# Optimization experiments

Hardware: AMD Instinct MI355X
Metric: run time of the kernel (lower is better)

The kernel has to match this reference:

```python
import jax, jax.numpy as jnp
import numpy as np

B, DK, N, DV = 16, 64, 8192, 64


def setup_inputs() -> dict:
    key = jax.random.key(0)
    kq, kk, kv = jax.random.split(key, 3)
    q = jax.random.normal(kq, (B, DK, N), dtype=jnp.float32)   # channel-first q
    k = jax.random.normal(kk, (B, N, DK), dtype=jnp.float32)
    v = jax.random.normal(kv, (B, N, DV), dtype=jnp.float32)
    return {"q": q, "k": k, "v": v}


def reference(q, k, v):
    # torch: bmm(q.permute(0,2,1), bmm(k.permute(0,2,1), v))
    # k^T v: [B, DK, DV] -- small on-chip-able intermediate
    ktv = jnp.einsum('bnk,bnv->bkv', k, v)
    # q^T (k^T v): [B, N, DV]
    out = jnp.einsum('bkn,bkv->bnv', q, ktv)
    return out
```

## Files before the change

### kernel.cpp

```cpp
#include <hip/hip_runtime.h>


#define B_   16
#define N_   8192
#define DK_  64
#define DV_  64
#define CH_  32

__global__ __launch_bounds__(256) void p1_partial(
    const float* __restrict__ K, const float* __restrict__ V,
    float* __restrict__ part)
{
    __shared__ float sm[4][4096];

    const int c = blockIdx.x, b = blockIdx.y, t = threadIdx.x;
    const int w = t >> 6, lane = t & 63;
    const int kk = (lane >> 3) * 8;
    const int vv = (lane & 7) * 8;

    float* Ks = &sm[w][0];
    float* Vs = &sm[w][2048];

    const size_t row0 = (size_t)b * N_ + (size_t)c * 256 + (size_t)w * 64;
    const float4* K4 = (const float4*)(K + row0 * DK_);
    const float4* V4 = (const float4*)(V + row0 * DV_);

    float acc[8][8] = {};

    for (int r = 0; r < 2; ++r) {
        #pragma unroll
        for (int j = 0; j < 8; ++j) {
            ((float4*)Ks)[lane + 64 * j] = K4[r * 512 + lane + 64 * j];
            ((float4*)Vs)[lane + 64 * j] = V4[r * 512 + lane + 64 * j];
        }
        #pragma unroll 4
        for (int n = 0; n < 32; ++n) {
            alignas(16) float fk[8], fv[8];
            *(float4*)&fk[0] = *(const float4*)&Ks[n * 64 + kk];
            *(float4*)&fk[4] = *(const float4*)&Ks[n * 64 + kk + 4];
            *(float4*)&fv[0] = *(const float4*)&Vs[n * 64 + vv];
            *(float4*)&fv[4] = *(const float4*)&Vs[n * 64 + vv + 4];
            #pragma unroll
            for (int i = 0; i < 8; ++i)
                #pragma unroll
                for (int j = 0; j < 8; ++j)
                    acc[i][j] += fk[i] * fv[j];
        }
    }

    float* reg = sm[w];
    #pragma unroll
    for (int i = 0; i < 8; ++i) {
        *(float4*)&reg[(kk + i) * 64 + vv]     = make_float4(acc[i][0], acc[i][1], acc[i][2], acc[i][3]);
        *(float4*)&reg[(kk + i) * 64 + vv + 4] = make_float4(acc[i][4], acc[i][5], acc[i][6], acc[i][7]);
    }
    __syncthreads();

    float4* P = (float4*)(part + ((size_t)c * B_ + b) * 4096);
    #pragma unroll
    for (int j = 0; j < 4; ++j) {
        const int idx = t + 256 * j;
        const float4 s0 = ((const float4*)sm[0])[idx];
        const float4 s1 = ((const float4*)sm[1])[idx];
        const float4 s2 = ((const float4*)sm[2])[idx];
        const float4 s3 = ((const float4*)sm[3])[idx];
        P[idx] = make_float4(s0.x + s1.x + s2.x + s3.x,
                             s0.y + s1.y + s2.y + s3.y,
                             s0.z + s1.z + s2.z + s3.z,
                             s0.w + s1.w + s2.w + s3.w);
    }
}

__global__ __launch_bounds__(256) void p1_reduce(
    const float* __restrict__ part, float* __restrict__ ktv)
{
    const int idx = blockIdx.x * 256 + threadIdx.x;
    float s = 0.f;
    #pragma unroll
    for (int c = 0; c < CH_; ++c)
        s += part[(size_t)c * 65536 + idx];
    ktv[idx] = s;
}

__global__ __launch_bounds__(256) void p2(
    const float* __restrict__ q, const float* __restrict__ ktv,
    float* __restrict__ out)
{
    __shared__ float ks[4096];
    __shared__ float qs[4][4096];

    const int nb = blockIdx.x, b = blockIdx.y, t = threadIdx.x;
    const int w = t >> 6, lane = t & 63;
    const int nl = (lane >> 3) * 8;
    const int vl = (lane & 7) * 8;
    const int n0 = nb * 256 + w * 64;

    const float4* kt4 = (const float4*)(ktv + (size_t)b * 4096);
    #pragma unroll
    for (int j = 0; j < 4; ++j)
        ((float4*)ks)[t + 256 * j] = kt4[t + 256 * j];

    const float* qb = q + (size_t)b * DK_ * N_ + n0;
    #pragma unroll
    for (int j = 0; j < 16; ++j) {
        const int idx = lane + 64 * j;
        ((float4*)qs[w])[idx] =
            ((const float4*)(qb + (size_t)(idx >> 4) * N_))[idx & 15];
    }
    __syncthreads();

    float acc[8][8] = {};
    #pragma unroll 8
    for (int k = 0; k < 64; ++k) {
        alignas(16) float fq[8], fv[8];
        *(float4*)&fq[0] = *(const float4*)&qs[w][k * 64 + nl];
        *(float4*)&fq[4] = *(const float4*)&qs[w][k * 64 + nl + 4];
        *(float4*)&fv[0] = *(const float4*)&ks[k * 64 + vl];
        *(float4*)&fv[4] = *(const float4*)&ks[k * 64 + vl + 4];
        #pragma unroll
        for (int i = 0; i < 8; ++i)
            #pragma unroll
            for (int j = 0; j < 8; ++j)
                acc[i][j] += fq[i] * fv[j];
    }

    float* ob = out + ((size_t)b * N_ + n0 + nl) * DV_ + vl;
    #pragma unroll
    for (int i = 0; i < 8; ++i) {
        *(float4*)&ob[(size_t)i * DV_]     = make_float4(acc[i][0], acc[i][1], acc[i][2], acc[i][3]);
        *(float4*)&ob[(size_t)i * DV_ + 4] = make_float4(acc[i][4], acc[i][5], acc[i][6], acc[i][7]);
    }
}

extern "C" void kernel_launch(void* const* d_in, const int* in_sizes, int n_in,
                              void* d_out, int out_size, void* d_ws, size_t ws_size,
                              hipStream_t stream)
{
    (void)in_sizes; (void)n_in; (void)out_size; (void)ws_size;
    const float* q = (const float*)d_in[0];
    const float* k = (const float*)d_in[1];
    const float* v = (const float*)d_in[2];
    float* out = (float*)d_out;

    float* part = (float*)d_ws;
    float* ktv  = part + (size_t)CH_ * B_ * 4096;

    p1_partial<<<dim3(CH_, B_), 256, 0, stream>>>(k, v, part);
    p1_reduce<<<dim3(256), 256, 0, stream>>>(part, ktv);
    p2<<<dim3(32, B_), 256, 0, stream>>>(q, ktv, out);
}
```

Measured before the change: 151.7 us.

## Use direct global-to-LDS loads with double buffering to overlap loads and FMA

Replaces register-staged global-to-shared copies with global_load_lds DMA builtins in both the K^T V partial kernel and the q-projection kernel. The partial kernel is split into four 16-row chunks with two LDS buffers, so the next chunk's loads are issued while the current one is computed. In p2 the second half of q is loaded after the barrier and overlaps the first half of the k-loop. The goal is to hide global memory latency and free registers. Correctness now relies on manual vmcnt waits and on the fixed per-lane LDS placement of the DMA builtin, which is fragile.

Result: no change. 152.3 us (+0.4%).

```diff
diff --git a/kernel.cpp b/kernel.cpp
--- a/kernel.cpp
+++ b/kernel.cpp
@@ -6,6 +6,13 @@
 #define DK_  64
 #define DV_  64
 #define CH_  32
+
+__device__ __forceinline__ void dma16(const void* g, void* l) {
+    __builtin_amdgcn_global_load_lds(
+        (const __attribute__((address_space(1))) void*)g,
+        (__attribute__((address_space(3))) void*)l, 16, 0, 0);
+}
+#define WAITVM(n) __builtin_amdgcn_s_waitcnt(0x0F70 | (n))
 
 __global__ __launch_bounds__(256) void p1_partial(
     const float* __restrict__ K, const float* __restrict__ V,
@@ -17,42 +24,55 @@
     const int w = t >> 6, lane = t & 63;
     const int kk = (lane >> 3) * 8;
     const int vv = (lane & 7) * 8;
-
-    float* Ks = &sm[w][0];
-    float* Vs = &sm[w][2048];
+    float* wsm = sm[w];
 
     const size_t row0 = (size_t)b * N_ + (size_t)c * 256 + (size_t)w * 64;
     const float4* K4 = (const float4*)(K + row0 * DK_);
     const float4* V4 = (const float4*)(V + row0 * DV_);
 
+    #pragma unroll
+    for (int r = 0; r < 2; ++r)
+        #pragma unroll
+        for (int j = 0; j < 4; ++j) {
+            dma16(&K4[r * 256 + j * 64 + lane], &wsm[(r & 1) * 2048 + j * 256]);
+            dma16(&V4[r * 256 + j * 64 + lane], &wsm[(r & 1) * 2048 + 1024 + j * 256]);
+        }
+
     float acc[8][8] = {};
 
-    for (int r = 0; r < 2; ++r) {
-        #pragma unroll
-        for (int j = 0; j < 8; ++j) {
-            ((float4*)Ks)[lane + 64 * j] = K4[r * 512 + lane + 64 * j];
-            ((float4*)Vs)[lane + 64 * j] = V4[r * 512 + lane + 64 * j];
-        }
-        #pragma unroll 4
-        for (int n = 0; n < 32; ++n) {
+    #pragma unroll
+    for (int r = 0; r < 4; ++r) {
+        if (r < 3) WAITVM(8);
+        else       WAITVM(0);
+        const float* Kb = &wsm[(r & 1) * 2048];
+        const float* Vb = &wsm[(r & 1) * 2048 + 1024];
+        #pragma unroll 8
+        for (int n = 0; n < 16; ++n) {
             alignas(16) float fk[8], fv[8];
-            *(float4*)&fk[0] = *(const float4*)&Ks[n * 64 + kk];
-            *(float4*)&fk[4] = *(const float4*)&Ks[n * 64 + kk + 4];
-            *(float4*)&fv[0] = *(const float4*)&Vs[n * 64 + vv];
-            *(float4*)&fv[4] = *(const float4*)&Vs[n * 64 + vv + 4];
+            *(float4*)&fk[0] = *(const float4*)&Kb[n * 64 + kk];
+            *(float4*)&fk[4] = *(const float4*)&Kb[n * 64 + kk + 4];
+            *(float4*)&fv[0] = *(const float4*)&Vb[n * 64 + vv];
+            *(float4*)&fv[4] = *(const float4*)&Vb[n * 64 + vv + 4];
             #pragma unroll
             for (int i = 0; i < 8; ++i)
                 #pragma unroll
                 for (int j = 0; j < 8; ++j)
                     acc[i][j] += fk[i] * fv[j];
         }
+        if (r + 2 < 4) {
+            const int rn = r + 2;
+            #pragma unroll
+            for (int j = 0; j < 4; ++j) {
+                dma16(&K4[rn * 256 + j * 64 + lane], &wsm[(rn & 1) * 2048 + j * 256]);
+                dma16(&V4[rn * 256 + j * 64 + lane], &wsm[(rn & 1) * 2048 + 1024 + j * 256]);
+            }
+        }
     }
 
-    float* reg = sm[w];
     #pragma unroll
     for (int i = 0; i < 8; ++i) {
-        *(float4*)&reg[(kk + i) * 64 + vv]     = make_float4(acc[i][0], acc[i][1], acc[i][2], acc[i][3]);
-        *(float4*)&reg[(kk + i) * 64 + vv + 4] = make_float4(acc[i][4], acc[i][5], acc[i][6], acc[i][7]);
+        *(float4*)&wsm[(kk + i) * 64 + vv]     = make_float4(acc[i][0], acc[i][1], acc[i][2], acc[i][3]);
+        *(float4*)&wsm[(kk + i) * 64 + vv + 4] = make_float4(acc[i][4], acc[i][5], acc[i][6], acc[i][7]);
     }
     __syncthreads();
 
@@ -94,27 +114,46 @@
     const int nl = (lane >> 3) * 8;
     const int vl = (lane & 7) * 8;
     const int n0 = nb * 256 + w * 64;
+    float* qsw = qs[w];
 
     const float4* kt4 = (const float4*)(ktv + (size_t)b * 4096);
     #pragma unroll
     for (int j = 0; j < 4; ++j)
-        ((float4*)ks)[t + 256 * j] = kt4[t + 256 * j];
+        dma16(&kt4[w * 256 + j * 64 + lane], &ks[w * 1024 + j * 256]);
 
     const float* qb = q + (size_t)b * DK_ * N_ + n0;
     #pragma unroll
-    for (int j = 0; j < 16; ++j) {
-        const int idx = lane + 64 * j;
-        ((float4*)qs[w])[idx] =
-            ((const float4*)(qb + (size_t)(idx >> 4) * N_))[idx & 15];
-    }
+    for (int j = 0; j < 8; ++j)
+        dma16(qb + (size_t)(4 * j + (lane >> 4)) * N_ + (lane & 15) * 4,
+              &qsw[j * 256]);
+
     __syncthreads();
+
+    #pragma unroll
+    for (int j = 8; j < 16; ++j)
+        dma16(qb + (size_t)(4 * j + (lane >> 4)) * N_ + (lane & 15) * 4,
+              &qsw[j * 256]);
 
     float acc[8][8] = {};
     #pragma unroll 8
-    for (int k = 0; k < 64; ++k) {
+    for (int k = 0; k < 32; ++k) {
         alignas(16) float fq[8], fv[8];
-        *(float4*)&fq[0] = *(const float4*)&qs[w][k * 64 + nl];
-        *(float4*)&fq[4] = *(const float4*)&qs[w][k * 64 + nl + 4];
+        *(float4*)&fq[0] = *(const float4*)&qsw[k * 64 + nl];
+        *(float4*)&fq[4] = *(const float4*)&qsw[k * 64 + nl + 4];
+        *(float4*)&fv[0] = *(const float4*)&ks[k * 64 + vl];
+        *(float4*)&fv[4] = *(const float4*)&ks[k * 64 + vl + 4];
+        #pragma unroll
+        for (int i = 0; i < 8; ++i)
+            #pragma unroll
+            for (int j = 0; j < 8; ++j)
+                acc[i][j] += fq[i] * fv[j];
+    }
+    WAITVM(0);
+    #pragma unroll 8
+    for (int k = 32; k < 64; ++k) {
+        alignas(16) float fq[8], fv[8];
+        *(float4*)&fq[0] = *(const float4*)&qsw[k * 64 + nl];
+        *(float4*)&fq[4] = *(const float4*)&qsw[k * 64 + nl + 4];
         *(float4*)&fv[0] = *(const float4*)&ks[k * 64 + vl];
         *(float4*)&fv[4] = *(const float4*)&ks[k * 64 + vl + 4];
         #pragma unroll
```

## Drop LDS staging, load operands directly from global, double grid sizes

Applied to the files above, without the earlier changes.

Both kernels now read K/V and q/ktv directly from global memory into registers instead of staging them through shared memory. The per-block chunk shrinks (128 rows), which doubles the block count for both p1_partial and p2, and p2 computes a 4x8 tile per thread. The cross-wave reduction in p1_partial uses a single 16KB LDS buffer accumulated serially with barriers. This cuts LDS footprint to raise occupancy and parallelism. In exchange it doubles the partial-sum traffic handled by p1_reduce and relies on the cache for the repeated, non-coalesced per-thread global loads.

Result: slower. 203.5 us (+34.1%).

```diff
diff --git a/kernel.cpp b/kernel.cpp
--- a/kernel.cpp
+++ b/kernel.cpp
@@ -5,70 +5,66 @@
 #define N_   8192
 #define DK_  64
 #define DV_  64
-#define CH_  32
+#define CH_  64
 
 __global__ __launch_bounds__(256) void p1_partial(
     const float* __restrict__ K, const float* __restrict__ V,
     float* __restrict__ part)
 {
-    __shared__ float sm[4][4096];
+    __shared__ float red[4096];
 
     const int c = blockIdx.x, b = blockIdx.y, t = threadIdx.x;
     const int w = t >> 6, lane = t & 63;
     const int kk = (lane >> 3) * 8;
     const int vv = (lane & 7) * 8;
 
-    float* Ks = &sm[w][0];
-    float* Vs = &sm[w][2048];
-
-    const size_t row0 = (size_t)b * N_ + (size_t)c * 256 + (size_t)w * 64;
-    const float4* K4 = (const float4*)(K + row0 * DK_);
-    const float4* V4 = (const float4*)(V + row0 * DV_);
+    const size_t row0 = (size_t)b * N_ + (size_t)c * 128 + (size_t)w * 32;
+    const float* Kl = K + row0 * DK_ + kk;
+    const float* Vl = V + row0 * DV_ + vv;
 
     float acc[8][8] = {};
+    #pragma unroll 4
+    for (int n = 0; n < 32; ++n) {
+        alignas(16) float fk[8], fv[8];
+        *(float4*)&fk[0] = *(const float4*)(Kl + n * 64);
+        *(float4*)&fk[4] = *(const float4*)(Kl + n * 64 + 4);
+        *(float4*)&fv[0] = *(const float4*)(Vl + n * 64);
+        *(float4*)&fv[4] = *(const float4*)(Vl + n * 64 + 4);
+        #pragma unroll
+        for (int i = 0; i < 8; ++i)
+            #pragma unroll
+            for (int j = 0; j < 8; ++j)
+                acc[i][j] += fk[i] * fv[j];
+    }
 
-    for (int r = 0; r < 2; ++r) {
+    if (w == 0) {
         #pragma unroll
-        for (int j = 0; j < 8; ++j) {
-            ((float4*)Ks)[lane + 64 * j] = K4[r * 512 + lane + 64 * j];
-            ((float4*)Vs)[lane + 64 * j] = V4[r * 512 + lane + 64 * j];
-        }
-        #pragma unroll 4
-        for (int n = 0; n < 32; ++n) {
-            alignas(16) float fk[8], fv[8];
-            *(float4*)&fk[0] = *(const float4*)&Ks[n * 64 + kk];
-            *(float4*)&fk[4] = *(const float4*)&Ks[n * 64 + kk + 4];
-            *(float4*)&fv[0] = *(const float4*)&Vs[n * 64 + vv];
-            *(float4*)&fv[4] = *(const float4*)&Vs[n * 64 + vv + 4];
-            #pragma unroll
-            for (int i = 0; i < 8; ++i)
-                #pragma unroll
-                for (int j = 0; j < 8; ++j)
-                    acc[i][j] += fk[i] * fv[j];
+        for (int i = 0; i < 8; ++i) {
+            *(float4*)&red[(kk + i) * 64 + vv]     = make_float4(acc[i][0], acc[i][1], acc[i][2], acc[i][3]);
+            *(float4*)&red[(kk + i) * 64 + vv + 4] = make_float4(acc[i][4], acc[i][5], acc[i][6], acc[i][7]);
         }
     }
-
-    float* reg = sm[w];
+    __syncthreads();
     #pragma unroll
-    for (int i = 0; i < 8; ++i) {
-        *(float4*)&reg[(kk + i) * 64 + vv]     = make_float4(acc[i][0], acc[i][1], acc[i][2], acc[i][3]);
-        *(float4*)&reg[(kk + i) * 64 + vv + 4] = make_float4(acc[i][4], acc[i][5], acc[i][6], acc[i][7]);
+    for (int ww = 1; ww < 4; ++ww) {
+        if (w == ww) {
+            #pragma unroll
+            for (int i = 0; i < 8; ++i) {
+                float4 r0 = *(float4*)&red[(kk + i) * 64 + vv];
+                float4 r1 = *(float4*)&red[(kk + i) * 64 + vv + 4];
+                r0.x += acc[i][0]; r0.y += acc[i][1]; r0.z += acc[i][2]; r0.w += acc[i][3];
+                r1.x += acc[i][4]; r1.y += acc[i][5]; r1.z += acc[i][6]; r1.w += acc[i][7];
+                *(float4*)&red[(kk + i) * 64 + vv]     = r0;
+                *(float4*)&red[(kk + i) * 64 + vv + 4] = r1;
+            }
+        }
+        __syncthreads();
     }
-    __syncthreads();
 
     float4* P = (float4*)(part + ((size_t)c * B_ + b) * 4096);
     #pragma unroll
-    for (int j = 0; j < 4; ++j) {
-        const int idx = t + 256 * j;
-        const float4 s0 = ((const float4*)sm[0])[idx];
-        const float4 s1 = ((const float4*)sm[1])[idx];
-        const float4 s2 = ((const float4*)sm[2])[idx];
-        const float4 s3 = ((const float4*)sm[3])[idx];
-        P[idx] = make_float4(s0.x + s1.x + s2.x + s3.x,
-                             s0.y + s1.y + s2.y + s3.y,
-                             s0.z + s1.z + s2.z + s3.z,
-                             s0.w + s1.w + s2.w + s3.w);
-    }
+    for (int j = 0; j < 4; ++j)
+        P[t + 256 * j] = ((const float4*)red)[t + 256 * j];
 }
 
 __global__ __launch_bounds__(256) void p1_reduce(
@@ -86,39 +82,24 @@
     const float* __restrict__ q, const float* __restrict__ ktv,
     float* __restrict__ out)
 {
-    __shared__ float ks[4096];
-    __shared__ float qs[4][4096];
-
     const int nb = blockIdx.x, b = blockIdx.y, t = threadIdx.x;
     const int w = t >> 6, lane = t & 63;
-    const int nl = (lane >> 3) * 8;
+    const int nl = (lane >> 3) * 4;
     const int vl = (lane & 7) * 8;
-    const int n0 = nb * 256 + w * 64;
+    const int n0 = nb * 128 + w * 32;
 
-    const float4* kt4 = (const float4*)(ktv + (size_t)b * 4096);
-    #pragma unroll
-    for (int j = 0; j < 4; ++j)
-        ((float4*)ks)[t + 256 * j] = kt4[t + 256 * j];
+    const float* ql = q + (size_t)b * DK_ * N_ + n0 + nl;
+    const float* kl = ktv + (size_t)b * 4096 + vl;
 
-    const float* qb = q + (size_t)b * DK_ * N_ + n0;
-    #pragma unroll
-    for (int j = 0; j < 16; ++j) {
-        const int idx = lane + 64 * j;
-        ((float4*)qs[w])[idx] =
-            ((const float4*)(qb + (size_t)(idx >> 4) * N_))[idx & 15];
-    }
-    __syncthreads();
-
-    float acc[8][8] = {};
-    #pragma unroll 8
+    float acc[4][8] = {};
+    #pragma unroll 4
     for (int k = 0; k < 64; ++k) {
-        alignas(16) float fq[8], fv[8];
-        *(float4*)&fq[0] = *(const float4*)&qs[w][k * 64 + nl];
-        *(float4*)&fq[4] = *(const float4*)&qs[w][k * 64 + nl + 4];
-        *(float4*)&fv[0] = *(const float4*)&ks[k * 64 + vl];
-        *(float4*)&fv[4] = *(const float4*)&ks[k * 64 + vl + 4];
+        alignas(16) float fq[4], fv[8];
+        *(float4*)&fq[0] = *(const float4*)(ql + (size_t)k * N_);
+        *(float4*)&fv[0] = *(const float4*)(kl + k * 64);
+        *(float4*)&fv[4] = *(const float4*)(kl + k * 64 + 4);
         #pragma unroll
-        for (int i = 0; i < 8; ++i)
+        for (int i = 0; i < 4; ++i)
             #pragma unroll
             for (int j = 0; j < 8; ++j)
                 acc[i][j] += fq[i] * fv[j];
@@ -126,7 +107,7 @@
 
     float* ob = out + ((size_t)b * N_ + n0 + nl) * DV_ + vl;
     #pragma unroll
-    for (int i = 0; i < 8; ++i) {
+    for (int i = 0; i < 4; ++i) {
         *(float4*)&ob[(size_t)i * DV_]     = make_float4(acc[i][0], acc[i][1], acc[i][2], acc[i][3]);
         *(float4*)&ob[(size_t)i * DV_ + 4] = make_float4(acc[i][4], acc[i][5], acc[i][6], acc[i][7]);
     }
@@ -147,5 +128,5 @@
 
     p1_partial<<<dim3(CH_, B_), 256, 0, stream>>>(k, v, part);
     p1_reduce<<<dim3(256), 256, 0, stream>>>(part, ktv);
-    p2<<<dim3(32, B_), 256, 0, stream>>>(q, ktv, out);
+    p2<<<dim3(64, B_), 256, 0, stream>>>(q, ktv, out);
 }
```
